# Kernel tuning notes

Hardware: AMD Instinct MI355X
Metric: run time of the kernel (lower is better)

The kernel has to match this reference:

```python
import jax, jax.numpy as jnp
import numpy as np

N = 100000        # num nodes
F_IN = 256        # params['topo_feature']
C = 128           # params['num_edge'] (hidden & GCN channels)
E = 1_600_000     # num edges (avg degree 16)


def setup_inputs() -> dict:
    key = jax.random.key(0)
    k = jax.random.split(key, 6)
    x = jax.random.normal(k[0], (N, F_IN), dtype=jnp.float32)
    edge_index = jax.random.randint(k[1], (2, E), 0, N, dtype=jnp.int32)
    # fc1: Linear(F_IN, C)
    W1 = jax.random.normal(k[2], (C, F_IN), dtype=jnp.float32) * (1.0 / np.sqrt(F_IN))
    b1 = jnp.zeros((C,), dtype=jnp.float32)
    # GCNConv linear: Linear(C, C, bias=False) weight + separate bias added post-aggregation
    W2 = jax.random.normal(k[3], (C, C), dtype=jnp.float32) * (1.0 / np.sqrt(C))
    b2 = jnp.zeros((C,), dtype=jnp.float32)
    return {"x": x, "edge_index": edge_index, "W1": W1, "b1": b1, "W2": W2, "b2": b2}


def reference(x, edge_index, W1, b1, W2, b2):
    # fc1 + relu
    h = jax.nn.relu(x @ W1.T + b1)                       # [N, C]
    # GCNConv: transform, add self-loops, sym-normalize, scatter-add
    z = h @ W2.T                                         # [N, C]
    loop = jnp.arange(N, dtype=edge_index.dtype)
    src = jnp.concatenate([edge_index[0], loop])         # [E+N]
    dst = jnp.concatenate([edge_index[1], loop])         # [E+N]
    deg = jax.ops.segment_sum(jnp.ones_like(dst, jnp.float32), dst, num_segments=N)
    dinv = jnp.where(deg > 0, jax.lax.rsqrt(jnp.maximum(deg, 1.0)), 0.0)
    norm = (dinv[src] * dinv[dst])[:, None]              # [E+N, 1]
    out = jax.ops.segment_sum(z[src] * norm, dst, num_segments=N) + b2
    return out
```

## Files before the change

### kernel.cpp

```cpp
#include <hip/hip_runtime.h>

typedef unsigned short ushort;
typedef __bf16 bf16x8 __attribute__((ext_vector_type(8)));
typedef float f32x4 __attribute__((ext_vector_type(4)));

#define F_IN 256
#define CCH  128
#define BSH  7
#define BNODES 128
#define NBUCK 1024
#define CHUNK 2048

__device__ __forceinline__ ushort f2bf(float f) {
    union { float f; unsigned i; } u; u.f = f;
    unsigned r = u.i + 0x7fffu + ((u.i >> 16) & 1u);
    return (ushort)(r >> 16);
}
__device__ __forceinline__ float2 bf2f2(unsigned u) {
    union { unsigned i; float f; } lo, hi;
    lo.i = u << 16;
    hi.i = u & 0xffff0000u;
    return make_float2(lo.f, hi.f);
}
__device__ __forceinline__ void gload_lds16(const void* g, void* l) {
    __builtin_amdgcn_global_load_lds((const __attribute__((address_space(1))) unsigned*)g,
                                     (__attribute__((address_space(3))) unsigned*)l, 16, 0, 0);
}

__global__ __launch_bounds__(256)
void hist_cvt(const int* __restrict__ dst, int* __restrict__ histC, int* __restrict__ histT,
              int E, int nchunks, int ncp,
              const float* __restrict__ W1, const float* __restrict__ W2,
              ushort* __restrict__ w1b, ushort* __restrict__ w2b)
{
    const int blk = blockIdx.x, t = threadIdx.x;
    if (blk >= nchunks) {
        int i = (blk - nchunks) * 256 + t;
        if (i < CCH * F_IN) {
            int c  = i & 31;
            int cs = c ^ (((i >> 9) & 3) << 3);
            w1b[(i & ~31) | cs] = f2bf(W1[i]);
        } else {
            int j = i - CCH * F_IN;
            if (j < CCH * CCH) w2b[j] = f2bf(W2[j]);
        }
        return;
    }
    __shared__ int h[NBUCK];
    for (int i = t; i < NBUCK; i += 256) h[i] = 0;
    __syncthreads();
    int cb = blk * CHUNK, ce = min(cb + CHUNK, E);
    for (int e = cb + t; e < ce; e += 256)
        atomicAdd(&h[dst[e] >> BSH], 1);
    __syncthreads();
    const int ncp16 = ncp * 16;
    for (int i = t; i < NBUCK; i += 256) {
        int v = h[i];
        histC[blk * NBUCK + i] = v;
        histT[(i >> 4) * ncp16 + blk * 16 + (i & 15)] = v;
    }
}

__global__ __launch_bounds__(256)
void scan_buckets(const int* __restrict__ histT, int* __restrict__ prefT,
                  int* __restrict__ btot, int nchunks, int ncp)
{
    const int b = blockIdx.x * 4 + (threadIdx.x >> 6);
    const int lane = threadIdx.x & 63;
    const int tbase = (b >> 4) * (ncp * 16) + (b & 15);
    int carry = 0;
    for (int c = 0; c < nchunks; c += 64) {
        int idx = c + lane;
        int v = (idx < nchunks) ? histT[tbase + idx * 16] : 0;
        int inc = v;
#pragma unroll
        for (int off = 1; off < 64; off <<= 1) {
            int x = __shfl_up(inc, off, 64);
            if (lane >= off) inc += x;
        }
        if (idx < nchunks) prefT[b * ncp + idx] = carry + inc - v;
        carry += __shfl(inc, 63, 64);
    }
    if (lane == 0) btot[b] = carry;
}

__device__ __forceinline__ void partition_body(unsigned* smem4,
    const int* __restrict__ src, const int* __restrict__ dst,
    const int* __restrict__ histC, const int* __restrict__ prefT,
    const int* __restrict__ btot, int* __restrict__ gbase,
    unsigned* __restrict__ pairs, int E, int ncp, int blk)
{
    int* lbase  = (int*)smem4;
    int* lcur   = lbase + NBUCK;
    int* rb2    = lcur + NBUCK;
    int* base_s = rb2 + NBUCK;
    int* ssum   = base_s + NBUCK;
    unsigned* sp = (unsigned*)(ssum + 256);
    ushort* sb  = (ushort*)(sp + CHUNK);
    const int t = threadIdx.x;

    int4 cv = *(const int4*)&histC[blk * NBUCK + 4 * t];
    int tsum = cv.x + cv.y + cv.z + cv.w;
    ssum[t] = tsum;
    __syncthreads();
    for (int off = 1; off < 256; off <<= 1) {
        int x = (t >= off) ? ssum[t - off] : 0;
        __syncthreads();
        ssum[t] += x;
        __syncthreads();
    }
    int texcl = ssum[t] - tsum;
    lbase[4 * t]     = texcl;
    lbase[4 * t + 1] = texcl + cv.x;
    lbase[4 * t + 2] = texcl + cv.x + cv.y;
    lbase[4 * t + 3] = texcl + cv.x + cv.y + cv.z;
    lcur[4 * t]     = lbase[4 * t];
    lcur[4 * t + 1] = lbase[4 * t + 1];
    lcur[4 * t + 2] = lbase[4 * t + 2];
    lcur[4 * t + 3] = lbase[4 * t + 3];
    __syncthreads();

    int4 bt = *(const int4*)&btot[4 * t];
    int bsum = bt.x + bt.y + bt.z + bt.w;
    ssum[t] = bsum;
    __syncthreads();
    for (int off = 1; off < 256; off <<= 1) {
        int x = (t >= off) ? ssum[t - off] : 0;
        __syncthreads();
        ssum[t] += x;
        __syncthreads();
    }
    int bexcl = ssum[t] - bsum;
    base_s[4 * t]     = bexcl;
    base_s[4 * t + 1] = bexcl + bt.x;
    base_s[4 * t + 2] = bexcl + bt.x + bt.y;
    base_s[4 * t + 3] = bexcl + bt.x + bt.y + bt.z;
    if (blk == 0) {
        *(int4*)&gbase[4 * t] = *(int4*)&base_s[4 * t];
        if (t == 255) gbase[NBUCK] = ssum[255];
    }
    __syncthreads();
    for (int i = t; i < NBUCK; i += 256)
        rb2[i] = base_s[i] + prefT[i * ncp + blk];
    __syncthreads();

    const int cb = blk * CHUNK, ce = min(cb + CHUNK, E);
    for (int e = cb + t; e < ce; e += 256) {
        int d = dst[e];
        int b = d >> BSH;
        unsigned packed = ((unsigned)src[e] << BSH) | (unsigned)(d & (BNODES - 1));
        int p = atomicAdd(&lcur[b], 1);
        sp[p] = packed;
        sb[p] = (ushort)b;
    }
    __syncthreads();
    const int cnt = ce - cb;
    for (int i = t; i < cnt; i += 256) {
        int b = sb[i];
        pairs[rb2[b] + (i - lbase[b])] = sp[i];
    }
}

__device__ __forceinline__ void csr_body(unsigned* smem4,
    const unsigned* __restrict__ pairs, const int* __restrict__ base,
    int* __restrict__ row_start, float* __restrict__ dinv,
    unsigned* __restrict__ csr, int N, int E, int b, int lastb)
{
    int* deg = (int*)smem4;
    int* s   = deg + BNODES;
    int* cur = s + BNODES;
    const int t = threadIdx.x;
    if (t < BNODES) deg[t] = 0;
    __syncthreads();
    const int rb = base[b], re = base[b + 1];
    for (int e = rb + t; e < re; e += 256)
        atomicAdd(&deg[pairs[e] & (BNODES - 1)], 1);
    __syncthreads();
    int v = (t < BNODES) ? deg[t] : 0;
    if (t < BNODES) s[t] = v;
    __syncthreads();
    for (int off = 1; off < BNODES; off <<= 1) {
        int x = (t >= off && t < BNODES) ? s[t - off] : 0;
        __syncthreads();
        if (t < BNODES) s[t] += x;
        __syncthreads();
    }
    const int n0 = b << BSH;
    if (t < BNODES) {
        int excl = s[t] - v;
        cur[t] = excl;
        if (n0 + t < N) {
            row_start[n0 + t] = rb + excl;
            dinv[n0 + t] = rsqrtf((float)v + 1.0f);
        }
    }
    if (b == lastb && t == 0) row_start[N] = E;
    __syncthreads();
    for (int e = rb + t; e < re; e += 256) {
        unsigned p = pairs[e];
        int l = p & (BNODES - 1);
        int slot = atomicAdd(&cur[l], 1);
        csr[rb + slot] = p >> BSH;
    }
}

__device__ __forceinline__ void gemm_body(unsigned* smem4,
    const float* __restrict__ X, const ushort* __restrict__ W1b,
    const ushort* __restrict__ W2b, const float* __restrict__ b1,
    ushort* __restrict__ Zq, int M, int m0)
{
    ushort* smem = (ushort*)smem4;
    ushort* Ht = smem;
    const int tid  = threadIdx.x;
    const int wave = tid >> 6, lane = tid & 63;
    const int wm = (wave & 1) * 64, wn = (wave >> 1) * 64;
    const int lr = lane & 15, lq = lane >> 4;

    const int arow = tid >> 2;
    const int aq   = tid & 3;

    float4 ar[2][2];
    auto loadX = [&](int k0) {
#pragma unroll
        for (int it = 0; it < 2; it++) {
            int grow = min(m0 + arow + it * 64, M - 1);
            const float* p = &X[(long)grow * F_IN + k0 + aq * 8];
            ar[it][0] = *(const float4*)p;
            ar[it][1] = *(const float4*)(p + 4);
        }
    };
    auto writeA = [&](ushort* As) {
#pragma unroll
        for (int it = 0; it < 2; it++) {
            int row = arow + it * 64;
            ushort u[8] = { f2bf(ar[it][0].x), f2bf(ar[it][0].y), f2bf(ar[it][0].z), f2bf(ar[it][0].w),
                            f2bf(ar[it][1].x), f2bf(ar[it][1].y), f2bf(ar[it][1].z), f2bf(ar[it][1].w) };
            *(uint4*)&As[row * 32 + ((aq ^ ((row >> 1) & 3)) << 3)] = *(uint4*)u;
        }
    };
    auto stageB = [&](int k0, ushort* Bs) {
#pragma unroll
        for (int it = 0; it < 2; it++) {
            int r0 = wave * 32 + it * 16;
            const ushort* g = &W1b[(long)(r0 + (lane >> 2)) * F_IN + k0 + (lane & 3) * 8];
            gload_lds16(g, &Bs[r0 * 32]);
        }
    };

    f32x4 acc[4][4] = {};
    loadX(0);
    stageB(0, smem + 4096);
    writeA(smem);
    __syncthreads();
    for (int k0 = 0; k0 < F_IN; k0 += 32) {
        const int cur = (k0 >> 5) & 1;
        ushort* As = smem + cur * 8192;
        ushort* Bs = As + 4096;
        const bool more = (k0 + 32 < F_IN);
        if (more) {
            stageB(k0 + 32, smem + (cur ^ 1) * 8192 + 4096);
            loadX(k0 + 32);
        }
        bf16x8 af[4], bfr[4];
#pragma unroll
        for (int t4 = 0; t4 < 4; t4++) {
            int ra = wm + t4 * 16 + lr;
            int rb = wn + t4 * 16 + lr;
            af[t4]  = *(bf16x8*)&As[ra * 32 + ((lq ^ ((ra >> 1) & 3)) << 3)];
            bfr[t4] = *(bf16x8*)&Bs[rb * 32 + ((lq ^ ((rb >> 1) & 3)) << 3)];
        }
#pragma unroll
        for (int i = 0; i < 4; i++)
#pragma unroll
            for (int j = 0; j < 4; j++)
                acc[i][j] = __builtin_amdgcn_mfma_f32_16x16x32_bf16(af[i], bfr[j], acc[i][j], 0, 0, 0);
        if (more) writeA(smem + (cur ^ 1) * 8192);
        __syncthreads();
    }

    uint4 wb[2][4];
#pragma unroll
    for (int t4 = 0; t4 < 4; t4++)
        wb[0][t4] = *(const uint4*)&W2b[(long)(wn + t4 * 16 + lr) * CCH + lq * 8];

    {
        float bv[4];
#pragma unroll
        for (int j = 0; j < 4; j++) bv[j] = b1[wn + j * 16 + lr];
#pragma unroll
        for (int i = 0; i < 4; i++)
#pragma unroll
            for (int r = 0; r < 4; r++) {
                int row = wm + i * 16 + lq * 4 + r;
                int rx  = (row & 7) << 3;
#pragma unroll
                for (int j = 0; j < 4; j++)
                    Ht[row * 128 + ((wn + j * 16 + lr) ^ rx)] = f2bf(fmaxf(acc[i][j][r] + bv[j], 0.f));
            }
    }
    __syncthreads();

    f32x4 acc2[4][4] = {};
#pragma unroll
    for (int kk = 0; kk < 4; kk++) {
        const int k0 = kk * 32;
        if (kk < 3) {
#pragma unroll
            for (int t4 = 0; t4 < 4; t4++)
                wb[(kk + 1) & 1][t4] =
                    *(const uint4*)&W2b[(long)(wn + t4 * 16 + lr) * CCH + k0 + 32 + lq * 8];
        }
        bf16x8 af[4];
#pragma unroll
        for (int t4 = 0; t4 < 4; t4++) {
            int ra = wm + t4 * 16 + lr;
            af[t4] = *(bf16x8*)&Ht[ra * 128 + ((k0 + lq * 8) ^ ((ra & 7) << 3))];
        }
#pragma unroll
        for (int i = 0; i < 4; i++)
#pragma unroll
            for (int j = 0; j < 4; j++)
                acc2[i][j] = __builtin_amdgcn_mfma_f32_16x16x32_bf16(af[i], *(bf16x8*)&wb[kk & 1][j],
                                                                     acc2[i][j], 0, 0, 0);
    }
    __syncthreads();

#pragma unroll
    for (int i = 0; i < 4; i++)
#pragma unroll
        for (int r = 0; r < 4; r++) {
            int row = wm + i * 16 + lq * 4 + r;
            int rx  = (row & 7) << 3;
#pragma unroll
            for (int j = 0; j < 4; j++)
                Ht[row * 128 + ((wn + j * 16 + lr) ^ rx)] = f2bf(acc2[i][j][r]);
        }
    __syncthreads();
    {
        int colq = tid & 15, row0 = tid >> 4;
#pragma unroll
        for (int i = 0; i < 8; i++) {
            int row = row0 + i * 16;
            if (m0 + row < M)
                *(uint4*)&Zq[(long)(m0 + row) * CCH + colq * 8] =
                    *(uint4*)&Ht[row * 128 + ((colq * 8) ^ ((row & 7) << 3))];
        }
    }
}

__global__ __launch_bounds__(256)
void u_part_gemm(const int* __restrict__ src, const int* __restrict__ dst,
                 const int* __restrict__ histC, const int* __restrict__ prefT,
                 const int* __restrict__ btot, int* __restrict__ gbase,
                 unsigned* __restrict__ pairs, int E, int ncp, int nchunks,
                 const float* __restrict__ X, const ushort* __restrict__ W1b,
                 const ushort* __restrict__ W2b, const float* __restrict__ b1,
                 ushort* __restrict__ Zq, int M)
{
    __shared__ unsigned smem4[8192];
    const int bid = blockIdx.x;
    if (bid < nchunks) {
        const int x = bid & 7, i = bid >> 3;
        const int q = nchunks >> 3, r = nchunks & 7;
        const int chunk = (x < r) ? x * (q + 1) + i : r * (q + 1) + (x - r) * q + i;
        partition_body(smem4, src, dst, histC, prefT, btot, gbase, pairs, E, ncp, chunk);
    } else {
        gemm_body(smem4, X, W1b, W2b, b1, Zq, M, (bid - nchunks) * 128);
    }
}

__global__ __launch_bounds__(256)
void u_csr_gemm(const unsigned* __restrict__ pairs, const int* __restrict__ base,
                int* __restrict__ row_start, float* __restrict__ dinv,
                unsigned* __restrict__ csr, int N, int E, int nbuck, int ngA,
                const float* __restrict__ X, const ushort* __restrict__ W1b,
                const ushort* __restrict__ W2b, const float* __restrict__ b1,
                ushort* __restrict__ Zq, int M)
{
    __shared__ unsigned smem4[8192];
    const int bid = blockIdx.x;
    if (bid < nbuck)
        csr_body(smem4, pairs, base, row_start, dinv, csr, N, E, bid, nbuck - 1);
    else
        gemm_body(smem4, X, W1b, W2b, b1, Zq, M, (ngA + bid - nbuck) * 128);
}

__global__ __launch_bounds__(256)
void gather_nodes(const unsigned* __restrict__ zq, const unsigned* __restrict__ csr,
                  const int* __restrict__ row_start, const float* __restrict__ dinv,
                  const float* __restrict__ b2, float* __restrict__ out, int N)
{
    const int node = blockIdx.x * 4 + (threadIdx.x >> 6);
    const int lane = threadIdx.x & 63;
    if (node >= N) return;

    const float di = dinv[node];
    float2 zs = bf2f2(zq[(long)node * 64 + lane]);
    float acc0 = di * zs.x, acc1 = di * zs.y;

    const int rs = row_start[node];
    const int re = row_start[node + 1];
    int j = rs;
    for (; j + 8 <= re; j += 8) {
        unsigned sI[8], zv[8];
        float dv[8];
#pragma unroll
        for (int q = 0; q < 8; q++) sI[q] = csr[j + q];
#pragma unroll
        for (int q = 0; q < 8; q++) dv[q] = dinv[sI[q]];
#pragma unroll
        for (int q = 0; q < 8; q++) zv[q] = zq[(long)sI[q] * 64 + lane];
#pragma unroll
        for (int q = 0; q < 8; q++) { float2 f = bf2f2(zv[q]); acc0 += dv[q] * f.x; acc1 += dv[q] * f.y; }
    }
    for (; j < re; j++) {
        unsigned s = csr[j];
        float ds = dinv[s];
        float2 f = bf2f2(zq[(long)s * 64 + lane]);
        acc0 += ds * f.x; acc1 += ds * f.y;
    }

    float2 o;
    o.x = b2[lane * 2 + 0] + di * acc0;
    o.y = b2[lane * 2 + 1] + di * acc1;
    *(float2*)&out[(long)node * CCH + lane * 2] = o;
}

extern "C" void kernel_launch(void* const* d_in, const int* in_sizes, int n_in,
                              void* d_out, int out_size, void* d_ws, size_t ws_size,
                              hipStream_t stream)
{
    const float* x  = (const float*)d_in[0];
    const int*   ei = (const int*)d_in[1];
    const float* W1 = (const float*)d_in[2];
    const float* b1 = (const float*)d_in[3];
    const float* W2 = (const float*)d_in[4];
    const float* b2 = (const float*)d_in[5];
    float* out = (float*)d_out;

    const int N = in_sizes[0] / F_IN;
    const int E = in_sizes[1] / 2;
    const int* src = ei;
    const int* dst = ei + E;

    const int nchunks = (E + CHUNK - 1) / CHUNK;
    const int ncp     = (nchunks + 63) & ~63;
    const int nbuck   = (N + BNODES - 1) / BNODES;
    const int ngrid   = (N + 127) / 128;
    const int ngA     = (ngrid + 1) / 2;
    const int ngB     = ngrid - ngA;
    const int ncvt    = (CCH * F_IN + CCH * CCH + 255) / 256;

    char* ws = (char*)d_ws;
    ushort* zq    = (ushort*)ws;   ws += (size_t)N * CCH * 2;
    ushort* w1b   = (ushort*)ws;   ws += (size_t)CCH * F_IN * 2;
    ushort* w2b   = (ushort*)ws;   ws += (size_t)CCH * CCH * 2;
    unsigned* prs = (unsigned*)ws; ws += (size_t)E * 4;
    unsigned* csr = (unsigned*)ws; ws += (size_t)E * 4;
    int* rstart   = (int*)ws;      ws += ((size_t)N + 1) * 4;
    float* dinv   = (float*)ws;    ws += (size_t)N * 4;
    int* histC    = (int*)ws;      ws += (size_t)nchunks * NBUCK * 4;
    int* histT    = (int*)ws;      ws += (size_t)NBUCK * ncp * 4;
    int* prefT    = (int*)ws;      ws += (size_t)NBUCK * ncp * 4;
    int* btot     = (int*)ws;      ws += NBUCK * 4;
    int* gbase    = (int*)ws;      ws += (NBUCK + 1) * 4;

    hist_cvt<<<nchunks + ncvt, 256, 0, stream>>>(dst, histC, histT, E, nchunks, ncp, W1, W2, w1b, w2b);
    scan_buckets<<<NBUCK / 4, 256, 0, stream>>>(histT, prefT, btot, nchunks, ncp);
    u_part_gemm<<<nchunks + ngA, 256, 0, stream>>>(src, dst, histC, prefT, btot, gbase, prs,
                                                   E, ncp, nchunks, x, w1b, w2b, b1, zq, N);
    u_csr_gemm<<<nbuck + ngB, 256, 0, stream>>>(prs, gbase, rstart, dinv, csr, N, E,
                                                nbuck, ngA, x, w1b, w2b, b1, zq, N);
    gather_nodes<<<(N + 3) / 4, 256, 0, stream>>>((const unsigned*)zq, csr, rstart, dinv, b2, out, N);
}
```

Baseline: 314.5 us.

## Use wave-shuffle scans, scatter partition directly, scan in place, deepen gather unroll

```diff
diff --git a/kernel.cpp b/kernel.cpp
--- a/kernel.cpp
+++ b/kernel.cpp
@@ -61,24 +61,24 @@
     }
 }
 
-__global__ __launch_bounds__(256)
-void scan_buckets(const int* __restrict__ histT, int* __restrict__ prefT,
-                  int* __restrict__ btot, int nchunks, int ncp)
-{
-    const int b = blockIdx.x * 4 + (threadIdx.x >> 6);
+__global__ __launch_bounds__(1024)
+void scan_buckets(int* __restrict__ histT, int* __restrict__ btot, int nchunks, int ncp)
+{
+    const int w = threadIdx.x >> 6;
+    const int b = blockIdx.x * 16 + w;
     const int lane = threadIdx.x & 63;
-    const int tbase = (b >> 4) * (ncp * 16) + (b & 15);
+    const int tb = blockIdx.x * (ncp * 16) + w;
     int carry = 0;
     for (int c = 0; c < nchunks; c += 64) {
         int idx = c + lane;
-        int v = (idx < nchunks) ? histT[tbase + idx * 16] : 0;
+        int v = (idx < nchunks) ? histT[tb + idx * 16] : 0;
         int inc = v;
 #pragma unroll
         for (int off = 1; off < 64; off <<= 1) {
             int x = __shfl_up(inc, off, 64);
             if (lane >= off) inc += x;
         }
-        if (idx < nchunks) prefT[b * ncp + idx] = carry + inc - v;
+        if (idx < nchunks) histT[tb + idx * 16] = carry + inc - v;
         carry += __shfl(inc, 63, 64);
     }
     if (lane == 0) btot[b] = carry;
@@ -86,62 +86,58 @@
 
 __device__ __forceinline__ void partition_body(unsigned* smem4,
     const int* __restrict__ src, const int* __restrict__ dst,
-    const int* __restrict__ histC, const int* __restrict__ prefT,
+    const int* __restrict__ histC, const int* __restrict__ histPre,
     const int* __restrict__ btot, int* __restrict__ gbase,
     unsigned* __restrict__ pairs, int E, int ncp, int blk)
 {
-    int* lbase  = (int*)smem4;
-    int* lcur   = lbase + NBUCK;
-    int* rb2    = lcur + NBUCK;
-    int* base_s = rb2 + NBUCK;
-    int* ssum   = base_s + NBUCK;
-    unsigned* sp = (unsigned*)(ssum + 256);
-    ushort* sb  = (ushort*)(sp + CHUNK);
+    int* lcur = (int*)smem4;
+    int* off  = lcur + NBUCK;
+    int* wsum = off + NBUCK;
     const int t = threadIdx.x;
+    const int wv = t >> 6, lane = t & 63;
 
     int4 cv = *(const int4*)&histC[blk * NBUCK + 4 * t];
     int tsum = cv.x + cv.y + cv.z + cv.w;
-    ssum[t] = tsum;
-    __syncthreads();
-    for (int off = 1; off < 256; off <<= 1) {
-        int x = (t >= off) ? ssum[t - off] : 0;
-        __syncthreads();
-        ssum[t] += x;
-        __syncthreads();
-    }
-    int texcl = ssum[t] - tsum;
-    lbase[4 * t]     = texcl;
-    lbase[4 * t + 1] = texcl + cv.x;
-    lbase[4 * t + 2] = texcl + cv.x + cv.y;
-    lbase[4 * t + 3] = texcl + cv.x + cv.y + cv.z;
-    lcur[4 * t]     = lbase[4 * t];
-    lcur[4 * t + 1] = lbase[4 * t + 1];
-    lcur[4 * t + 2] = lbase[4 * t + 2];
-    lcur[4 * t + 3] = lbase[4 * t + 3];
-    __syncthreads();
+    int inc = tsum;
+#pragma unroll
+    for (int o = 1; o < 64; o <<= 1) {
+        int x = __shfl_up(inc, o, 64);
+        if (lane >= o) inc += x;
+    }
+    if (lane == 63) wsum[wv] = inc;
+    __syncthreads();
+    int woff = 0;
+    if (wv > 0) woff += wsum[0];
+    if (wv > 1) woff += wsum[1];
+    if (wv > 2) woff += wsum[2];
+    int l0 = woff + inc - tsum, l1 = l0 + cv.x, l2 = l1 + cv.y, l3 = l2 + cv.z;
+    lcur[4 * t] = l0; lcur[4 * t + 1] = l1; lcur[4 * t + 2] = l2; lcur[4 * t + 3] = l3;
 
     int4 bt = *(const int4*)&btot[4 * t];
     int bsum = bt.x + bt.y + bt.z + bt.w;
-    ssum[t] = bsum;
-    __syncthreads();
-    for (int off = 1; off < 256; off <<= 1) {
-        int x = (t >= off) ? ssum[t - off] : 0;
-        __syncthreads();
-        ssum[t] += x;
-        __syncthreads();
-    }
-    int bexcl = ssum[t] - bsum;
-    base_s[4 * t]     = bexcl;
-    base_s[4 * t + 1] = bexcl + bt.x;
-    base_s[4 * t + 2] = bexcl + bt.x + bt.y;
-    base_s[4 * t + 3] = bexcl + bt.x + bt.y + bt.z;
+    int binc = bsum;
+#pragma unroll
+    for (int o = 1; o < 64; o <<= 1) {
+        int x = __shfl_up(binc, o, 64);
+        if (lane >= o) binc += x;
+    }
+    __syncthreads();
+    if (lane == 63) wsum[wv] = binc;
+    __syncthreads();
+    int bwoff = 0;
+    if (wv > 0) bwoff += wsum[0];
+    if (wv > 1) bwoff += wsum[1];
+    if (wv > 2) bwoff += wsum[2];
+    int b0 = bwoff + binc - bsum, b1 = b0 + bt.x, b2 = b1 + bt.y, b3 = b2 + bt.z;
     if (blk == 0) {
-        *(int4*)&gbase[4 * t] = *(int4*)&base_s[4 * t];
-        if (t == 255) gbase[NBUCK] = ssum[255];
-    }
-    __syncthreads();
-    for (int i = t; i < NBUCK; i += 256)
-        rb2[i] = base_s[i] + prefT[i * ncp + blk];
+        *(int4*)&gbase[4 * t] = make_int4(b0, b1, b2, b3);
+        if (t == 255) gbase[NBUCK] = b3 + bt.w;
+    }
+    int4 pf = *(const int4*)&histPre[(t >> 2) * (ncp * 16) + blk * 16 + (t & 3) * 4];
+    off[4 * t]     = b0 + pf.x - l0;
+    off[4 * t + 1] = b1 + pf.y - l1;
+    off[4 * t + 2] = b2 + pf.z - l2;
+    off[4 * t + 3] = b3 + pf.w - l3;
     __syncthreads();
 
     const int cb = blk * CHUNK, ce = min(cb + CHUNK, E);
@@ -150,14 +146,7 @@
         int b = d >> BSH;
         unsigned packed = ((unsigned)src[e] << BSH) | (unsigned)(d & (BNODES - 1));
         int p = atomicAdd(&lcur[b], 1);
-        sp[p] = packed;
-        sb[p] = (ushort)b;
-    }
-    __syncthreads();
-    const int cnt = ce - cb;
-    for (int i = t; i < cnt; i += 256) {
-        int b = sb[i];
-        pairs[rb2[b] + (i - lbase[b])] = sp[i];
+        pairs[off[b] + p] = packed;
     }
 }
 
@@ -166,9 +155,9 @@
     int* __restrict__ row_start, float* __restrict__ dinv,
     unsigned* __restrict__ csr, int N, int E, int b, int lastb)
 {
-    int* deg = (int*)smem4;
-    int* s   = deg + BNODES;
-    int* cur = s + BNODES;
+    int* deg  = (int*)smem4;
+    int* cur  = deg + BNODES;
+    int* wsum = cur + BNODES;
     const int t = threadIdx.x;
     if (t < BNODES) deg[t] = 0;
     __syncthreads();
@@ -177,18 +166,18 @@
         atomicAdd(&deg[pairs[e] & (BNODES - 1)], 1);
     __syncthreads();
     int v = (t < BNODES) ? deg[t] : 0;
-    if (t < BNODES) s[t] = v;
-    __syncthreads();
-    for (int off = 1; off < BNODES; off <<= 1) {
-        int x = (t >= off && t < BNODES) ? s[t - off] : 0;
-        __syncthreads();
-        if (t < BNODES) s[t] += x;
-        __syncthreads();
-    }
+    int inc = v;
+#pragma unroll
+    for (int o = 1; o < 64; o <<= 1) {
+        int x = __shfl_up(inc, o, 64);
+        if ((t & 63) >= o) inc += x;
+    }
+    if (t < BNODES && (t & 63) == 63) wsum[t >> 6] = inc;
+    __syncthreads();
     const int n0 = b << BSH;
     if (t < BNODES) {
-        int excl = s[t] - v;
-        cur[t] = excl;
+        int excl = inc - v + ((t >= 64) ? wsum[0] : 0);
+        cur[t] = rb + excl;
         if (n0 + t < N) {
             row_start[n0 + t] = rb + excl;
             dinv[n0 + t] = rsqrtf((float)v + 1.0f);
@@ -198,9 +187,8 @@
     __syncthreads();
     for (int e = rb + t; e < re; e += 256) {
         unsigned p = pairs[e];
-        int l = p & (BNODES - 1);
-        int slot = atomicAdd(&cur[l], 1);
-        csr[rb + slot] = p >> BSH;
+        int slot = atomicAdd(&cur[p & (BNODES - 1)], 1);
+        csr[slot] = p >> BSH;
     }
 }
 
@@ -350,7 +338,7 @@
 
 __global__ __launch_bounds__(256)
 void u_part_gemm(const int* __restrict__ src, const int* __restrict__ dst,
-                 const int* __restrict__ histC, const int* __restrict__ prefT,
+                 const int* __restrict__ histC, const int* __restrict__ histPre,
                  const int* __restrict__ btot, int* __restrict__ gbase,
                  unsigned* __restrict__ pairs, int E, int ncp, int nchunks,
                  const float* __restrict__ X, const ushort* __restrict__ W1b,
@@ -363,7 +351,7 @@
         const int x = bid & 7, i = bid >> 3;
         const int q = nchunks >> 3, r = nchunks & 7;
         const int chunk = (x < r) ? x * (q + 1) + i : r * (q + 1) + (x - r) * q + i;
-        partition_body(smem4, src, dst, histC, prefT, btot, gbase, pairs, E, ncp, chunk);
+        partition_body(smem4, src, dst, histC, histPre, btot, gbase, pairs, E, ncp, chunk);
     } else {
         gemm_body(smem4, X, W1b, W2b, b1, Zq, M, (bid - nchunks) * 128);
     }
@@ -401,17 +389,29 @@
     const int rs = row_start[node];
     const int re = row_start[node + 1];
     int j = rs;
-    for (; j + 8 <= re; j += 8) {
-        unsigned sI[8], zv[8];
-        float dv[8];
-#pragma unroll
-        for (int q = 0; q < 8; q++) sI[q] = csr[j + q];
-#pragma unroll
-        for (int q = 0; q < 8; q++) dv[q] = dinv[sI[q]];
-#pragma unroll
-        for (int q = 0; q < 8; q++) zv[q] = zq[(long)sI[q] * 64 + lane];
-#pragma unroll
-        for (int q = 0; q < 8; q++) { float2 f = bf2f2(zv[q]); acc0 += dv[q] * f.x; acc1 += dv[q] * f.y; }
+    for (; j + 16 <= re; j += 16) {
+        unsigned sI[16], zv[16];
+        float dv[16];
+#pragma unroll
+        for (int q = 0; q < 16; q++) sI[q] = csr[j + q];
+#pragma unroll
+        for (int q = 0; q < 16; q++) zv[q] = zq[(long)sI[q] * 64 + lane];
+#pragma unroll
+        for (int q = 0; q < 16; q++) dv[q] = dinv[sI[q]];
+#pragma unroll
+        for (int q = 0; q < 16; q++) { float2 f = bf2f2(zv[q]); acc0 += dv[q] * f.x; acc1 += dv[q] * f.y; }
+    }
+    for (; j + 4 <= re; j += 4) {
+        unsigned sI[4], zv[4];
+        float dv[4];
+#pragma unroll
+        for (int q = 0; q < 4; q++) sI[q] = csr[j + q];
+#pragma unroll
+        for (int q = 0; q < 4; q++) zv[q] = zq[(long)sI[q] * 64 + lane];
+#pragma unroll
+        for (int q = 0; q < 4; q++) dv[q] = dinv[sI[q]];
+#pragma unroll
+        for (int q = 0; q < 4; q++) { float2 f = bf2f2(zv[q]); acc0 += dv[q] * f.x; acc1 += dv[q] * f.y; }
     }
     for (; j < re; j++) {
         unsigned s = csr[j];
@@ -461,13 +461,12 @@
     float* dinv   = (float*)ws;    ws += (size_t)N * 4;
     int* histC    = (int*)ws;      ws += (size_t)nchunks * NBUCK * 4;
     int* histT    = (int*)ws;      ws += (size_t)NBUCK * ncp * 4;
-    int* prefT    = (int*)ws;      ws += (size_t)NBUCK * ncp * 4;
     int* btot     = (int*)ws;      ws += NBUCK * 4;
     int* gbase    = (int*)ws;      ws += (NBUCK + 1) * 4;
 
     hist_cvt<<<nchunks + ncvt, 256, 0, stream>>>(dst, histC, histT, E, nchunks, ncp, W1, W2, w1b, w2b);
-    scan_buckets<<<NBUCK / 4, 256, 0, stream>>>(histT, prefT, btot, nchunks, ncp);
-    u_part_gemm<<<nchunks + ngA, 256, 0, stream>>>(src, dst, histC, prefT, btot, gbase, prs,
+    scan_buckets<<<NBUCK / 16, 1024, 0, stream>>>(histT, btot, nchunks, ncp);
+    u_part_gemm<<<nchunks + ngA, 256, 0, stream>>>(src, dst, histC, histT, btot, gbase, prs,
                                                    E, ncp, nchunks, x, w1b, w2b, b1, zq, N);
     u_csr_gemm<<<nbuck + ngB, 256, 0, stream>>>(prs, gbase, rstart, dinv, csr, N, E,
                                                 nbuck, ngA, x, w1b, w2b, b1, zq, N);
```

Measured after the change: 344.7 us. 1.1x slower.
